# Optimization experiments

Measured on AMD Instinct MI355X. Metric: run time of the kernel, lower is better.

## Reference

```python
import jax, jax.numpy as jnp
import numpy as np

INPUT, HIDDEN, CLASSES = 4096, 4096, 1000


def setup_inputs() -> dict:
    key = jax.random.key(0)
    kx, kw1, kb1, kw2, kb2 = jax.random.split(key, 5)
    return {
        "x": jax.random.normal(kx, (8192, INPUT), dtype=jnp.float32),
        "fc1_weight": jax.random.normal(kw1, (HIDDEN, INPUT), dtype=jnp.float32),
        "fc1_bias": jax.random.normal(kb1, (HIDDEN,), dtype=jnp.float32),
        "fc2_weight": jax.random.normal(kw2, (CLASSES, HIDDEN), dtype=jnp.float32),
        "fc2_bias": jax.random.normal(kb2, (CLASSES,), dtype=jnp.float32),
    }


def reference(x, fc1_weight, fc1_bias, fc2_weight, fc2_bias):
    # x: [B, INPUT] (module flattens; already flat here)
    hidden = jnp.einsum("bi,hi->bh", x, fc1_weight) + fc1_bias  # [B, H]
    activated = jax.nn.relu(hidden)
    logits = jnp.einsum("bh,ch->bc", activated, fc2_weight) + fc2_bias  # [B, C]
    return jax.nn.softmax(logits, axis=-1)
```

## Files before the change

### kernel.cpp

```cpp
#include <hip/hip_runtime.h>
#include <hip/hip_fp16.h>
#include <stdint.h>

typedef __attribute__((ext_vector_type(8)))  _Float16 f16x8;
typedef __attribute__((ext_vector_type(4)))  _Float16 f16x4;
typedef __attribute__((ext_vector_type(4)))  float    f32x4;

__device__ __forceinline__ void split4(const f32x4 v, f16x4 &h, f16x4 &l) {
    #pragma unroll
    for (int i = 0; i < 4; ++i) {
        float a = v[i];
        _Float16 hh = (_Float16)a;
        h[i] = hh;
        l[i] = (_Float16)(a - (float)hh);
    }
}

__global__ __launch_bounds__(256)
void split_rows(const float* __restrict__ src, _Float16* __restrict__ h,
                _Float16* __restrict__ l, int srcRows, long long total4)
{
    const long long stride = (long long)gridDim.x * blockDim.x;
    for (long long i = (long long)blockIdx.x * blockDim.x + threadIdx.x; i < total4; i += stride) {
        const long long e = i << 2;
        const int row = (int)(e >> 12);
        f16x4 hv = {}, lv = {};
        if (row < srcRows) {
            f32x4 v = *(const f32x4*)(src + e);
            split4(v, hv, lv);
        }
        *(f16x4*)(h + e) = hv;
        *(f16x4*)(l + e) = lv;
    }
}


#define BARRIER() __builtin_amdgcn_s_barrier()
#define SB0()     __builtin_amdgcn_sched_barrier(0)
#define MFMA16    __builtin_amdgcn_mfma_f32_16x16x32_f16
#define SGB       __builtin_amdgcn_sched_group_barrier

template<int N> __device__ __forceinline__ void VMCNT() {
    asm volatile("s_waitcnt vmcnt(%0)" :: "n"(N) : "memory");
    __builtin_amdgcn_sched_barrier(0);
}

__device__ __forceinline__ void gload16(const _Float16* g, _Float16* l) {
    __builtin_amdgcn_global_load_lds(
        (const __attribute__((address_space(1))) void*)g,
        (__attribute__((address_space(3))) void*)l, 16, 0, 0);
}

template<int MI, bool SPLITOUT, bool CHUNKSWZ>
__global__ __launch_bounds__(512, 2)
void gemm3_v11(const _Float16* __restrict__ Agh, const _Float16* __restrict__ Agl,
               const _Float16* __restrict__ Bgh, const _Float16* __restrict__ Bgl,
               const float* __restrict__ bias,
               _Float16* __restrict__ Oh, _Float16* __restrict__ Ol,
               float* __restrict__ Of, int ldo, int Nstore,
               int K, int nBN)
{
    extern __shared__ _Float16 lds[];
    constexpr int WROWS = MI * 16;
    constexpr int BM    = MI * 32;
    constexpr int CHA   = MI * 2;
    constexpr int PW    = (2*CHA + 32) / 8;
    constexpr int H1    = PW - CHA/8;
    constexpr int H2    = CHA / 8;
    constexpr int ALO   = CHA * 512;
    constexpr int BHO   = 2 * CHA * 512;
    constexpr int BUFS  = 2*CHA*512 + 16384;

    const int tid  = threadIdx.x;
    const int lane = tid & 63;
    const int wave = tid >> 6;
    const int wm = wave >> 2;
    const int wn = wave & 3;
    const int fr = lane & 15;
    const int fg = lane >> 4;

    int bm, bn;
    const int orig = blockIdx.x;
    if (CHUNKSWZ) {
        bm = ((orig & 7) << 2) | ((orig >> 3) & 3);
        bn = orig >> 5;
    } else {
        const int cpx  = gridDim.x >> 3;
        const int swzb = (orig & 7) * cpx + (orig >> 3);
        bn = swzb % nBN;
        bm = swzb / nBN;
    }
    const int m0 = bm * BM;
    const int n0 = bn * 256;

    const _Float16* gptr[8];
    int loff[8];
    #pragma unroll
    for (int i = 0; i < PW; ++i) {
        int p, q;
        if (i < H2 || i >= H1) {
            const bool hi = (i >= H1);
            const int  s  = hi ? (i - H1) : i;
            const int  j  = wave * H2 + s;
            p = j / (CHA / 2);
            const int v   = j % (CHA / 2);
            const int wmq = v / (MI / 2);
            const int wi  = v % (MI / 2);
            q = wmq * MI + (hi ? MI / 2 : 0) + wi;
        } else {
            q = (i - H2) + (wave & 3) * 4;
            p = 2 + (wave >> 2);
        }
        const int row = q*16 + (lane >> 2);
        const int gc  = (lane & 3) ^ ((row >> 1) & 3);
        const _Float16* plane = (p == 0) ? Agh : (p == 1) ? Agl : (p == 2) ? Bgh : Bgl;
        const size_t grow = (size_t)((p < 2) ? m0 : n0) + row;
        gptr[i] = plane + grow * (size_t)K + gc * 8;
        loff[i] = ((p < 2) ? p * ALO : BHO + (p - 2) * 8192) + q * 512;
    }

    const int swz8 = (fg ^ ((fr >> 1) & 3)) * 8;
    int aoff[MI], boff[4];
    #pragma unroll
    for (int mi = 0; mi < MI; ++mi) aoff[mi] = (wm*WROWS + mi*16 + fr)*32 + swz8;
    #pragma unroll
    for (int ni = 0; ni < 4; ++ni)  boff[ni] = BHO + (wn*64 + ni*16 + fr)*32 + swz8;

    f32x4 acc[MI][4] = {};

    #pragma unroll
    for (int i = 0; i < PW; ++i) { gload16(gptr[i], &lds[loff[i]]); gptr[i] += 32; }
    VMCNT<0>(); BARRIER(); SB0();

    const int NT = K >> 5;
    int bb = 0;

#define MFMA3(MIdx, NIdx, AH, AL, BH, BL) do {                               \
        acc[MIdx][NIdx] = MFMA16((AH), (BH), acc[MIdx][NIdx], 0, 0, 0);      \
        acc[MIdx][NIdx] = MFMA16((AH), (BL), acc[MIdx][NIdx], 0, 0, 0);      \
        acc[MIdx][NIdx] = MFMA16((AL), (BH), acc[MIdx][NIdx], 0, 0, 0);      \
    } while (0)

#define MFMA12(MIdx, AH, AL) do {                                        \
        acc[MIdx][0] = MFMA16((AH), bh0, acc[MIdx][0], 0, 0, 0);         \
        acc[MIdx][1] = MFMA16((AH), bh1, acc[MIdx][1], 0, 0, 0);         \
        acc[MIdx][2] = MFMA16((AH), bh2, acc[MIdx][2], 0, 0, 0);         \
        acc[MIdx][3] = MFMA16((AH), bh3, acc[MIdx][3], 0, 0, 0);         \
        acc[MIdx][0] = MFMA16((AH), bl0, acc[MIdx][0], 0, 0, 0);         \
        acc[MIdx][1] = MFMA16((AH), bl1, acc[MIdx][1], 0, 0, 0);         \
        acc[MIdx][2] = MFMA16((AH), bl2, acc[MIdx][2], 0, 0, 0);         \
        acc[MIdx][3] = MFMA16((AH), bl3, acc[MIdx][3], 0, 0, 0);         \
        acc[MIdx][0] = MFMA16((AL), bh0, acc[MIdx][0], 0, 0, 0);         \
        acc[MIdx][1] = MFMA16((AL), bh1, acc[MIdx][1], 0, 0, 0);         \
        acc[MIdx][2] = MFMA16((AL), bh2, acc[MIdx][2], 0, 0, 0);         \
        acc[MIdx][3] = MFMA16((AL), bh3, acc[MIdx][3], 0, 0, 0);         \
    } while (0)

#define STEP_BODY(STG)                                                            \
    do {                                                                          \
        if (STG) {                                                                \
            _Pragma("unroll")                                                     \
            for (int i = 0; i < PW; ++i) {                                        \
                gload16(gptr[i], &lds[nbuf + loff[i]]); gptr[i] += 32;            \
            }                                                                     \
        }                                                                         \
        f16x8 ah[2], al[2];                                                       \
        f16x8 bh0, bl0, bh1, bl1, bh2, bl2, bh3, bl3;                             \
                                   \
        bh0 = *(const f16x8*)&lds[bb + boff[0]];                                  \
        bl0 = *(const f16x8*)&lds[bb + 8192 + boff[0]];                           \
        bh1 = *(const f16x8*)&lds[bb + boff[1]];                                  \
        bl1 = *(const f16x8*)&lds[bb + 8192 + boff[1]];                           \
        ah[0] = *(const f16x8*)&lds[bb + aoff[0]];                                \
        al[0] = *(const f16x8*)&lds[bb + ALO + aoff[0]];                          \
        if (STG) SGB(0x010, PW, 0);                                               \
        SGB(0x100, 6, 0);                                                         \
        __builtin_amdgcn_s_setprio(1);                                            \
                                         \
        bh2 = *(const f16x8*)&lds[bb + boff[2]];                                  \
        bl2 = *(const f16x8*)&lds[bb + 8192 + boff[2]];                           \
        bh3 = *(const f16x8*)&lds[bb + boff[3]];                                  \
        bl3 = *(const f16x8*)&lds[bb + 8192 + boff[3]];                           \
        MFMA3(0, 0, ah[0], al[0], bh0, bl0);                                      \
        MFMA3(0, 1, ah[0], al[0], bh1, bl1);                                      \
        SGB(0x100, 4, 0);                                                         \
        SGB(0x008, 6, 0);                                                         \
                                            \
        ah[1] = *(const f16x8*)&lds[bb + aoff[1]];                                \
        al[1] = *(const f16x8*)&lds[bb + ALO + aoff[1]];                          \
        MFMA3(0, 2, ah[0], al[0], bh2, bl2);                                      \
        MFMA3(0, 3, ah[0], al[0], bh3, bl3);                                      \
        SGB(0x100, 2, 0);                                                         \
        SGB(0x008, 6, 0);                                                         \
                                        \
        _Pragma("unroll")                                                         \
        for (int mi = 1; mi < MI; ++mi) {                                         \
            if (mi < MI - 1) {                                                    \
                ah[(mi + 1) & 1] = *(const f16x8*)&lds[bb + aoff[mi + 1]];        \
                al[(mi + 1) & 1] = *(const f16x8*)&lds[bb + ALO + aoff[mi + 1]];  \
                SGB(0x100, 2, 0);                                                 \
            }                                                                     \
            MFMA12(mi, ah[mi & 1], al[mi & 1]);                                   \
            SGB(0x008, 12, 0);                                                    \
        }                                                                         \
        __builtin_amdgcn_s_setprio(0);                                            \
    } while (0)

    for (int t = 0; t < NT - 1; ++t) {
        const int nbuf = BUFS - bb;
        STEP_BODY(true);
        VMCNT<0>(); BARRIER(); SB0();
        bb = nbuf;
    }
    {
        const int nbuf = 0; (void)nbuf;
        STEP_BODY(false);
    }
#undef STEP_BODY
#undef MFMA12
#undef MFMA3

    #pragma unroll
    for (int ni = 0; ni < 4; ++ni) {
        const int n = n0 + wn*64 + ni*16 + fr;
        if (!SPLITOUT && n >= Nstore) continue;
        const float bv = bias[n];
        #pragma unroll
        for (int mi = 0; mi < MI; ++mi) {
            #pragma unroll
            for (int j = 0; j < 4; ++j) {
                const int m = m0 + wm*WROWS + mi*16 + fg*4 + j;
                float v = acc[mi][ni][j] + bv;
                if (SPLITOUT) {
                    v = fmaxf(v, 0.f);
                    const _Float16 hh = (_Float16)v;
                    Oh[(size_t)m * ldo + n] = hh;
                    Ol[(size_t)m * ldo + n] = (_Float16)(v - (float)hh);
                } else {
                    Of[(size_t)m * ldo + n] = v;
                }
            }
        }
    }
}

#define TILE_M 128
#define TILE_N 128
#define TILE_K 32
#define LDSK   40

template<bool RELU, bool NGUARD>
__global__ __launch_bounds__(256, 2)
void gemm_split3(const float* __restrict__ A, const float* __restrict__ B,
                 const float* __restrict__ bias, float* __restrict__ C,
                 int K, int ldc, int Nreal)
{
    __shared__ _Float16 Ah[TILE_M][LDSK];
    __shared__ _Float16 Al[TILE_M][LDSK];
    __shared__ _Float16 Bh[TILE_N][LDSK];
    __shared__ _Float16 Bl[TILE_N][LDSK];

    const int tid  = threadIdx.x;
    const int lane = tid & 63;
    const int wave = tid >> 6;
    const int wr   = wave >> 1;
    const int wc   = wave & 1;
    const int m0   = blockIdx.x * TILE_M;
    const int n0   = blockIdx.y * TILE_N;
    const int srow = tid >> 3;
    const int scol = (tid & 7) << 2;
    const int fr = lane & 15;
    const int fg = lane >> 4;

    f32x4 acc[4][4] = {};

    for (int kt = 0; kt < K; kt += TILE_K) {
        __syncthreads();
        #pragma unroll
        for (int p = 0; p < 4; ++p) {
            const int row = srow + p * 32;
            f32x4 v = *(const f32x4*)(A + (size_t)(m0 + row) * K + kt + scol);
            f16x4 hv, lv;
            split4(v, hv, lv);
            *(f16x4*)&Ah[row][scol] = hv;
            *(f16x4*)&Al[row][scol] = lv;
        }
        #pragma unroll
        for (int p = 0; p < 4; ++p) {
            const int row = srow + p * 32;
            f32x4 v = {0.f, 0.f, 0.f, 0.f};
            if (!NGUARD || (n0 + row) < Nreal)
                v = *(const f32x4*)(B + (size_t)(n0 + row) * K + kt + scol);
            f16x4 hv, lv;
            split4(v, hv, lv);
            *(f16x4*)&Bh[row][scol] = hv;
            *(f16x4*)&Bl[row][scol] = lv;
        }
        __syncthreads();

        f16x8 ah[4], al[4];
        #pragma unroll
        for (int mi = 0; mi < 4; ++mi) {
            const int r = wr * 64 + mi * 16 + fr;
            ah[mi] = *(const f16x8*)&Ah[r][fg * 8];
            al[mi] = *(const f16x8*)&Al[r][fg * 8];
        }
        #pragma unroll
        for (int ni = 0; ni < 4; ++ni) {
            const int r = wc * 64 + ni * 16 + fr;
            const f16x8 bh = *(const f16x8*)&Bh[r][fg * 8];
            const f16x8 bl = *(const f16x8*)&Bl[r][fg * 8];
            #pragma unroll
            for (int mi = 0; mi < 4; ++mi) {
                acc[mi][ni] = __builtin_amdgcn_mfma_f32_16x16x32_f16(ah[mi], bh, acc[mi][ni], 0, 0, 0);
                acc[mi][ni] = __builtin_amdgcn_mfma_f32_16x16x32_f16(ah[mi], bl, acc[mi][ni], 0, 0, 0);
                acc[mi][ni] = __builtin_amdgcn_mfma_f32_16x16x32_f16(al[mi], bh, acc[mi][ni], 0, 0, 0);
            }
        }
    }

    #pragma unroll
    for (int ni = 0; ni < 4; ++ni) {
        const int n = n0 + wc * 64 + ni * 16 + fr;
        if (NGUARD && n >= Nreal) continue;
        const float bv = bias[n];
        #pragma unroll
        for (int mi = 0; mi < 4; ++mi) {
            #pragma unroll
            for (int j = 0; j < 4; ++j) {
                const int m = m0 + wr * 64 + mi * 16 + fg * 4 + j;
                float val = acc[mi][ni][j] + bv;
                if (RELU) val = fmaxf(val, 0.f);
                C[(size_t)m * ldc + n] = val;
            }
        }
    }
}

__global__ __launch_bounds__(256)
void softmax_rows(float* __restrict__ out, int rows, int cols)
{
    const int lane = threadIdx.x & 63;
    const int row  = blockIdx.x * 4 + (threadIdx.x >> 6);
    if (row >= rows) return;
    float* p = out + (size_t)row * cols;

    float v[16];
    float mx = -3.4e38f;
    #pragma unroll
    for (int j = 0; j < 16; ++j) {
        const int c = lane + j * 64;
        v[j] = (c < cols) ? p[c] : -3.4e38f;
        mx = fmaxf(mx, v[j]);
    }
    #pragma unroll
    for (int off = 32; off > 0; off >>= 1)
        mx = fmaxf(mx, __shfl_xor(mx, off));

    float s = 0.f;
    #pragma unroll
    for (int j = 0; j < 16; ++j) {
        const int c = lane + j * 64;
        const float e = (c < cols) ? __expf(v[j] - mx) : 0.f;
        v[j] = e;
        s += e;
    }
    #pragma unroll
    for (int off = 32; off > 0; off >>= 1)
        s += __shfl_xor(s, off);

    const float inv = 1.f / s;
    #pragma unroll
    for (int j = 0; j < 16; ++j) {
        const int c = lane + j * 64;
        if (c < cols) p[c] = v[j] * inv;
    }
}

extern "C" void kernel_launch(void* const* d_in, const int* in_sizes, int n_in,
                              void* d_out, int out_size, void* d_ws, size_t ws_size,
                              hipStream_t stream)
{
    const float* x  = (const float*)d_in[0];
    const float* w1 = (const float*)d_in[1];
    const float* b1 = (const float*)d_in[2];
    const float* w2 = (const float*)d_in[3];
    const float* b2 = (const float*)d_in[4];
    float* out = (float*)d_out;

    const size_t SZ_X  = (size_t)8192 * 4096 * 2;
    const size_t SZ_W1 = (size_t)4096 * 4096 * 2;
    const size_t SZ_W2 = (size_t)1024 * 4096 * 2;

    size_t off = 0;
    auto take = [&](size_t b) { size_t o = off; off += (b + 255) & ~(size_t)255; return o; };
    const size_t o_xh  = take(SZ_X),  o_xl  = take(SZ_X);
    const size_t o_w1h = take(SZ_W1), o_w1l = take(SZ_W1);
    const size_t o_w2h = take(SZ_W2), o_w2l = take(SZ_W2);
    const size_t o_ah  = take(SZ_X),  o_al  = take(SZ_X);
    const size_t need = off;

    bool attr_ok =
        (hipFuncSetAttribute((const void*)gemm3_v11<8, true, true>,
                             hipFuncAttributeMaxDynamicSharedMemorySize, 131072) == hipSuccess) &&
        (hipFuncSetAttribute((const void*)gemm3_v11<4, false, false>,
                             hipFuncAttributeMaxDynamicSharedMemorySize, 131072) == hipSuccess);

    const dim3 blk256(256, 1, 1), blk512(512, 1, 1);

    if (attr_ok && ws_size >= need) {
        char* w = (char*)d_ws;
        _Float16 *xh  = (_Float16*)(w + o_xh),  *xl  = (_Float16*)(w + o_xl);
        _Float16 *w1h = (_Float16*)(w + o_w1h), *w1l = (_Float16*)(w + o_w1l);
        _Float16 *w2h = (_Float16*)(w + o_w2h), *w2l = (_Float16*)(w + o_w2l);
        _Float16 *ath = (_Float16*)(w + o_ah),  *atl = (_Float16*)(w + o_al);

        hipLaunchKernelGGL(split_rows, dim3(2048), blk256, 0, stream, x,  xh,  xl,  8192, (long long)8192 * 1024);
        hipLaunchKernelGGL(split_rows, dim3(2048), blk256, 0, stream, w1, w1h, w1l, 4096, (long long)4096 * 1024);
        hipLaunchKernelGGL(split_rows, dim3(1024), blk256, 0, stream, w2, w2h, w2l, 1000, (long long)1024 * 1024);

        hipLaunchKernelGGL((gemm3_v11<8, true, true>), dim3(512), blk512, 131072, stream,
                           xh, xl, w1h, w1l, b1, ath, atl, (float*)nullptr, 4096, 4096, 4096, 16);
        hipLaunchKernelGGL((gemm3_v11<4, false, false>), dim3(256), blk512, 98304, stream,
                           ath, atl, w2h, w2l, b2, (_Float16*)nullptr, (_Float16*)nullptr,
                           out, 1000, 1000, 4096, 4);
        hipLaunchKernelGGL(softmax_rows, dim3(2048), blk256, 0, stream, out, 8192, 1000);
    } else {
        float* act = (float*)d_ws;
        hipLaunchKernelGGL((gemm_split3<true, false>), dim3(64, 32), blk256, 0, stream,
                           x, w1, b1, act, 4096, 4096, 4096);
        hipLaunchKernelGGL((gemm_split3<false, true>), dim3(64, 8), blk256, 0, stream,
                           act, w2, b2, out, 4096, 1000, 1000);
        hipLaunchKernelGGL(softmax_rows, dim3(2048), blk256, 0, stream, out, 8192, 1000);
    }
}
```

Measured before the change: 935.3 us.

## Load B operand fragments directly from global into registers, bypassing LDS

The B tiles (hi/lo fp16 weight planes) are no longer staged through LDS. Each wave now loads its own B fragments straight from global memory into double-buffered registers, one k-step ahead. Only the A tiles still go through LDS, which cuts LDS footprint and LDS read traffic and shrinks the dynamic shared memory request. In exchange, launch bounds drop to one block per CU so the extra B registers fit, which lowers occupancy. The per-wave B reads are also less coalesced and are shared less across waves, so more global and L2 traffic is possible.

New measurement: 1.393 ms. +48.9%, slower.

```diff
diff --git a/kernel.cpp b/kernel.cpp
--- a/kernel.cpp
+++ b/kernel.cpp
@@ -52,8 +52,8 @@
 }
 
 template<int MI, bool SPLITOUT, bool CHUNKSWZ>
-__global__ __launch_bounds__(512, 2)
-void gemm3_v11(const _Float16* __restrict__ Agh, const _Float16* __restrict__ Agl,
+__global__ __launch_bounds__(512, 1)
+void gemm3_v12(const _Float16* __restrict__ Agh, const _Float16* __restrict__ Agl,
                const _Float16* __restrict__ Bgh, const _Float16* __restrict__ Bgl,
                const float* __restrict__ bias,
                _Float16* __restrict__ Oh, _Float16* __restrict__ Ol,
@@ -63,13 +63,10 @@
     extern __shared__ _Float16 lds[];
     constexpr int WROWS = MI * 16;
     constexpr int BM    = MI * 32;
-    constexpr int CHA   = MI * 2;
-    constexpr int PW    = (2*CHA + 32) / 8;
-    constexpr int H1    = PW - CHA/8;
-    constexpr int H2    = CHA / 8;
-    constexpr int ALO   = CHA * 512;
-    constexpr int BHO   = 2 * CHA * 512;
-    constexpr int BUFS  = 2*CHA*512 + 16384;
+    constexpr int CH1   = BM / 16;
+    constexpr int PWA   = 2 * CH1 / 8;
+    constexpr int ALO   = BM * 32;
+    constexpr int BUFS  = 2 * ALO;
 
     const int tid  = threadIdx.x;
     const int lane = tid & 63;
@@ -93,132 +90,104 @@
     const int m0 = bm * BM;
     const int n0 = bn * 256;
 
-    const _Float16* gptr[8];
-    int loff[8];
-    #pragma unroll
-    for (int i = 0; i < PW; ++i) {
-        int p, q;
-        if (i < H2 || i >= H1) {
-            const bool hi = (i >= H1);
-            const int  s  = hi ? (i - H1) : i;
-            const int  j  = wave * H2 + s;
-            p = j / (CHA / 2);
-            const int v   = j % (CHA / 2);
-            const int wmq = v / (MI / 2);
-            const int wi  = v % (MI / 2);
-            q = wmq * MI + (hi ? MI / 2 : 0) + wi;
-        } else {
-            q = (i - H2) + (wave & 3) * 4;
-            p = 2 + (wave >> 2);
-        }
+    const _Float16* gptrA[PWA];
+    int loffA[PWA];
+    #pragma unroll
+    for (int i = 0; i < PWA; ++i) {
+        const int c = wave * PWA + i;
+        const int p = c / CH1;
+        const int q = c % CH1;
         const int row = q*16 + (lane >> 2);
         const int gc  = (lane & 3) ^ ((row >> 1) & 3);
-        const _Float16* plane = (p == 0) ? Agh : (p == 1) ? Agl : (p == 2) ? Bgh : Bgl;
-        const size_t grow = (size_t)((p < 2) ? m0 : n0) + row;
-        gptr[i] = plane + grow * (size_t)K + gc * 8;
-        loff[i] = ((p < 2) ? p * ALO : BHO + (p - 2) * 8192) + q * 512;
+        const _Float16* plane = p ? Agl : Agh;
+        gptrA[i] = plane + ((size_t)m0 + row) * (size_t)K + gc * 8;
+        loffA[i] = p * ALO + q * 512;
     }
 
     const int swz8 = (fg ^ ((fr >> 1) & 3)) * 8;
-    int aoff[MI], boff[4];
+    int aoff[MI];
     #pragma unroll
     for (int mi = 0; mi < MI; ++mi) aoff[mi] = (wm*WROWS + mi*16 + fr)*32 + swz8;
-    #pragma unroll
-    for (int ni = 0; ni < 4; ++ni)  boff[ni] = BHO + (wn*64 + ni*16 + fr)*32 + swz8;
-
+
+    const _Float16* gBh[4];
+    const _Float16* gBl[4];
+    #pragma unroll
+    for (int ni = 0; ni < 4; ++ni) {
+        const size_t row = (size_t)n0 + wn*64 + ni*16 + fr;
+        gBh[ni] = Bgh + row * (size_t)K + fg * 8;
+        gBl[ni] = Bgl + row * (size_t)K + fg * 8;
+    }
+
+    f16x8 breg_h[2][4], breg_l[2][4];
     f32x4 acc[MI][4] = {};
 
     #pragma unroll
-    for (int i = 0; i < PW; ++i) { gload16(gptr[i], &lds[loff[i]]); gptr[i] += 32; }
+    for (int i = 0; i < PWA; ++i) { gload16(gptrA[i], &lds[loffA[i]]); gptrA[i] += 32; }
+    #pragma unroll
+    for (int ni = 0; ni < 4; ++ni) {
+        breg_h[0][ni] = *(const f16x8*)gBh[ni]; gBh[ni] += 32;
+        breg_l[0][ni] = *(const f16x8*)gBl[ni]; gBl[ni] += 32;
+    }
     VMCNT<0>(); BARRIER(); SB0();
 
     const int NT = K >> 5;
     int bb = 0;
 
-#define MFMA3(MIdx, NIdx, AH, AL, BH, BL) do {                               \
-        acc[MIdx][NIdx] = MFMA16((AH), (BH), acc[MIdx][NIdx], 0, 0, 0);      \
-        acc[MIdx][NIdx] = MFMA16((AH), (BL), acc[MIdx][NIdx], 0, 0, 0);      \
-        acc[MIdx][NIdx] = MFMA16((AL), (BH), acc[MIdx][NIdx], 0, 0, 0);      \
+#define MFMA12(MIdx, AH, AL, BC) do {                                            \
+        acc[MIdx][0] = MFMA16((AH), breg_h[BC][0], acc[MIdx][0], 0, 0, 0);       \
+        acc[MIdx][1] = MFMA16((AH), breg_h[BC][1], acc[MIdx][1], 0, 0, 0);       \
+        acc[MIdx][2] = MFMA16((AH), breg_h[BC][2], acc[MIdx][2], 0, 0, 0);       \
+        acc[MIdx][3] = MFMA16((AH), breg_h[BC][3], acc[MIdx][3], 0, 0, 0);       \
+        acc[MIdx][0] = MFMA16((AH), breg_l[BC][0], acc[MIdx][0], 0, 0, 0);       \
+        acc[MIdx][1] = MFMA16((AH), breg_l[BC][1], acc[MIdx][1], 0, 0, 0);       \
+        acc[MIdx][2] = MFMA16((AH), breg_l[BC][2], acc[MIdx][2], 0, 0, 0);       \
+        acc[MIdx][3] = MFMA16((AH), breg_l[BC][3], acc[MIdx][3], 0, 0, 0);       \
+        acc[MIdx][0] = MFMA16((AL), breg_h[BC][0], acc[MIdx][0], 0, 0, 0);       \
+        acc[MIdx][1] = MFMA16((AL), breg_h[BC][1], acc[MIdx][1], 0, 0, 0);       \
+        acc[MIdx][2] = MFMA16((AL), breg_h[BC][2], acc[MIdx][2], 0, 0, 0);       \
+        acc[MIdx][3] = MFMA16((AL), breg_h[BC][3], acc[MIdx][3], 0, 0, 0);       \
     } while (0)
 
-#define MFMA12(MIdx, AH, AL) do {                                        \
-        acc[MIdx][0] = MFMA16((AH), bh0, acc[MIdx][0], 0, 0, 0);         \
-        acc[MIdx][1] = MFMA16((AH), bh1, acc[MIdx][1], 0, 0, 0);         \
-        acc[MIdx][2] = MFMA16((AH), bh2, acc[MIdx][2], 0, 0, 0);         \
-        acc[MIdx][3] = MFMA16((AH), bh3, acc[MIdx][3], 0, 0, 0);         \
-        acc[MIdx][0] = MFMA16((AH), bl0, acc[MIdx][0], 0, 0, 0);         \
-        acc[MIdx][1] = MFMA16((AH), bl1, acc[MIdx][1], 0, 0, 0);         \
-        acc[MIdx][2] = MFMA16((AH), bl2, acc[MIdx][2], 0, 0, 0);         \
-        acc[MIdx][3] = MFMA16((AH), bl3, acc[MIdx][3], 0, 0, 0);         \
-        acc[MIdx][0] = MFMA16((AL), bh0, acc[MIdx][0], 0, 0, 0);         \
-        acc[MIdx][1] = MFMA16((AL), bh1, acc[MIdx][1], 0, 0, 0);         \
-        acc[MIdx][2] = MFMA16((AL), bh2, acc[MIdx][2], 0, 0, 0);         \
-        acc[MIdx][3] = MFMA16((AL), bh3, acc[MIdx][3], 0, 0, 0);         \
-    } while (0)
-
-#define STEP_BODY(STG)                                                            \
+#define STEP_BODY(BC, BN_, STG)                                                   \
     do {                                                                          \
         if (STG) {                                                                \
             _Pragma("unroll")                                                     \
-            for (int i = 0; i < PW; ++i) {                                        \
-                gload16(gptr[i], &lds[nbuf + loff[i]]); gptr[i] += 32;            \
+            for (int i = 0; i < PWA; ++i) {                                       \
+                gload16(gptrA[i], &lds[nbuf + loffA[i]]); gptrA[i] += 32;         \
+            }                                                                     \
+            _Pragma("unroll")                                                     \
+            for (int ni = 0; ni < 4; ++ni) {                                      \
+                breg_h[BN_][ni] = *(const f16x8*)gBh[ni]; gBh[ni] += 32;          \
+                breg_l[BN_][ni] = *(const f16x8*)gBl[ni]; gBl[ni] += 32;          \
             }                                                                     \
         }                                                                         \
         f16x8 ah[2], al[2];                                                       \
-        f16x8 bh0, bl0, bh1, bl1, bh2, bl2, bh3, bl3;                             \
-                                   \
-        bh0 = *(const f16x8*)&lds[bb + boff[0]];                                  \
-        bl0 = *(const f16x8*)&lds[bb + 8192 + boff[0]];                           \
-        bh1 = *(const f16x8*)&lds[bb + boff[1]];                                  \
-        bl1 = *(const f16x8*)&lds[bb + 8192 + boff[1]];                           \
         ah[0] = *(const f16x8*)&lds[bb + aoff[0]];                                \
         al[0] = *(const f16x8*)&lds[bb + ALO + aoff[0]];                          \
-        if (STG) SGB(0x010, PW, 0);                                               \
-        SGB(0x100, 6, 0);                                                         \
+        if (STG) SGB(0x010, PWA + 8, 0);                                          \
+        SGB(0x100, 2, 0);                                                         \
         __builtin_amdgcn_s_setprio(1);                                            \
-                                         \
-        bh2 = *(const f16x8*)&lds[bb + boff[2]];                                  \
-        bl2 = *(const f16x8*)&lds[bb + 8192 + boff[2]];                           \
-        bh3 = *(const f16x8*)&lds[bb + boff[3]];                                  \
-        bl3 = *(const f16x8*)&lds[bb + 8192 + boff[3]];                           \
-        MFMA3(0, 0, ah[0], al[0], bh0, bl0);                                      \
-        MFMA3(0, 1, ah[0], al[0], bh1, bl1);                                      \
-        SGB(0x100, 4, 0);                                                         \
-        SGB(0x008, 6, 0);                                                         \
-                                            \
-        ah[1] = *(const f16x8*)&lds[bb + aoff[1]];                                \
-        al[1] = *(const f16x8*)&lds[bb + ALO + aoff[1]];                          \
-        MFMA3(0, 2, ah[0], al[0], bh2, bl2);                                      \
-        MFMA3(0, 3, ah[0], al[0], bh3, bl3);                                      \
-        SGB(0x100, 2, 0);                                                         \
-        SGB(0x008, 6, 0);                                                         \
-                                        \
         _Pragma("unroll")                                                         \
-        for (int mi = 1; mi < MI; ++mi) {                                         \
+        for (int mi = 0; mi < MI; ++mi) {                                         \
             if (mi < MI - 1) {                                                    \
                 ah[(mi + 1) & 1] = *(const f16x8*)&lds[bb + aoff[mi + 1]];        \
                 al[(mi + 1) & 1] = *(const f16x8*)&lds[bb + ALO + aoff[mi + 1]];  \
                 SGB(0x100, 2, 0);                                                 \
             }                                                                     \
-            MFMA12(mi, ah[mi & 1], al[mi & 1]);                                   \
+            MFMA12(mi, ah[mi & 1], al[mi & 1], BC);                               \
             SGB(0x008, 12, 0);                                                    \
         }                                                                         \
         __builtin_amdgcn_s_setprio(0);                                            \
     } while (0)
 
-    for (int t = 0; t < NT - 1; ++t) {
-        const int nbuf = BUFS - bb;
-        STEP_BODY(true);
-        VMCNT<0>(); BARRIER(); SB0();
-        bb = nbuf;
-    }
-    {
-        const int nbuf = 0; (void)nbuf;
-        STEP_BODY(false);
-    }
+    for (int it = 0; it < (NT - 2) / 2; ++it) {
+        { const int nbuf = BUFS - bb; STEP_BODY(0, 1, true); VMCNT<0>(); BARRIER(); SB0(); bb = nbuf; }
+        { const int nbuf = BUFS - bb; STEP_BODY(1, 0, true); VMCNT<0>(); BARRIER(); SB0(); bb = nbuf; }
+    }
+    { const int nbuf = BUFS - bb; STEP_BODY(0, 1, true); VMCNT<0>(); BARRIER(); SB0(); bb = nbuf; }
+    { const int nbuf = 0; (void)nbuf; STEP_BODY(1, 0, false); }
 #undef STEP_BODY
 #undef MFMA12
-#undef MFMA3
 
     #pragma unroll
     for (int ni = 0; ni < 4; ++ni) {
@@ -401,10 +370,10 @@
     const size_t need = off;
 
     bool attr_ok =
-        (hipFuncSetAttribute((const void*)gemm3_v11<8, true, true>,
-                             hipFuncAttributeMaxDynamicSharedMemorySize, 131072) == hipSuccess) &&
-        (hipFuncSetAttribute((const void*)gemm3_v11<4, false, false>,
-                             hipFuncAttributeMaxDynamicSharedMemorySize, 131072) == hipSuccess);
+        (hipFuncSetAttribute((const void*)gemm3_v12<8, true, true>,
+                             hipFuncAttributeMaxDynamicSharedMemorySize, 65536) == hipSuccess) &&
+        (hipFuncSetAttribute((const void*)gemm3_v12<4, false, false>,
+                             hipFuncAttributeMaxDynamicSharedMemorySize, 32768) == hipSuccess);
 
     const dim3 blk256(256, 1, 1), blk512(512, 1, 1);
 
@@ -419,9 +388,9 @@
         hipLaunchKernelGGL(split_rows, dim3(2048), blk256, 0, stream, w1, w1h, w1l, 4096, (long long)4096 * 1024);
         hipLaunchKernelGGL(split_rows, dim3(1024), blk256, 0, stream, w2, w2h, w2l, 1000, (long long)1024 * 1024);
 
-        hipLaunchKernelGGL((gemm3_v11<8, true, true>), dim3(512), blk512, 131072, stream,
+        hipLaunchKernelGGL((gemm3_v12<8, true, true>), dim3(512), blk512, 65536, stream,
                            xh, xl, w1h, w1l, b1, ath, atl, (float*)nullptr, 4096, 4096, 4096, 16);
-        hipLaunchKernelGGL((gemm3_v11<4, false, false>), dim3(256), blk512, 98304, stream,
+        hipLaunchKernelGGL((gemm3_v12<4, false, false>), dim3(256), blk512, 32768, stream,
                            ath, atl, w2h, w2l, b2, (_Float16*)nullptr, (_Float16*)nullptr,
                            out, 1000, 1000, 4096, 4);
         hipLaunchKernelGGL(softmax_rows, dim3(2048), blk256, 0, stream, out, 8192, 1000);
```
